# Optimization experiments

Hardware: AMD Instinct MI355X
Metric: run time of the kernel (lower is better)

The kernel has to match this reference:

```python
import jax, jax.numpy as jnp
import numpy as np

NUM_HEAD = 8
HIDDEN = 128
INPUT_DIM = 256
N1 = 1024
N2 = 1024
BATCH = 16


def setup_inputs() -> dict:
    key = jax.random.key(0)
    ks = jax.random.split(key, 10)
    HD = HIDDEN * NUM_HEAD  # 1024
    return {
        "x1": jax.random.normal(ks[0], (BATCH, N1, INPUT_DIM), jnp.float32),
        "x2": jax.random.normal(ks[1], (BATCH, N2, INPUT_DIM), jnp.float32),
        "B": jax.random.normal(ks[2], (N1, N2), jnp.float32),
        "wq_w": jax.random.normal(ks[3], (HD, INPUT_DIM), jnp.float32) * 0.02,
        "wq_b": jnp.zeros((HD,), jnp.float32),
        "wk_w": jax.random.normal(ks[4], (HD, INPUT_DIM), jnp.float32) * 0.02,
        "wk_b": jnp.zeros((HD,), jnp.float32),
        "wv_w": jax.random.normal(ks[5], (HD, INPUT_DIM), jnp.float32) * 0.02,
        "wv_b": jnp.zeros((HD,), jnp.float32),
        "proj_w": jax.random.normal(ks[6], (HIDDEN, HD), jnp.float32) * 0.02,
        "proj_b": jnp.zeros((HIDDEN,), jnp.float32),
    }


def reference(x1, x2, B, wq_w, wq_b, wk_w, wk_b, wv_w, wv_b, proj_w, proj_b):
    b, n1, _ = x1.shape
    n2 = x2.shape[1]
    sdk = jnp.sqrt(jnp.asarray(HIDDEN, x1.dtype))
    # Linear layers (torch convention: y = x @ W.T + b)
    q = x1 @ wq_w.T + wq_b                      # [b, n1, H*D]
    k = x2 @ wk_w.T + wk_b                      # [b, n2, H*D]
    v = x2 @ wv_w.T + wv_b                      # [b, n2, H*D]
    q = q.reshape(b, n1, NUM_HEAD, HIDDEN)
    k = k.reshape(b, n2, NUM_HEAD, HIDDEN)
    v = v.reshape(b, n2, NUM_HEAD, HIDDEN)
    # scores: [b, h, n1, n2]
    scores = jnp.einsum("bnhd,bmhd->bhnm", q, k) / sdk + B[None, None, :, :]
    attn = jax.nn.softmax(scores, axis=-1)
    out = jnp.einsum("bhnm,bmhd->bnhd", attn, v).reshape(b, n1, NUM_HEAD * HIDDEN)
    return out @ proj_w.T + proj_b              # [b, n1, HIDDEN]
```

## Files before the change

### kernel.cpp

```cpp
#include <hip/hip_runtime.h>
#include <hip/hip_fp16.h>

typedef _Float16 f16;
typedef __attribute__((ext_vector_type(4))) _Float16 f16x4;
typedef __attribute__((ext_vector_type(8))) _Float16 f16x8;
typedef __attribute__((ext_vector_type(4))) float f32x4;

#define MFMA_F16(a,b,c) __builtin_amdgcn_mfma_f32_16x16x32_f16((a),(b),(c),0,0,0)

__device__ __forceinline__ void gl_lds16(const f16* g, f16* l) {
  __builtin_amdgcn_global_load_lds(
      (const __attribute__((address_space(1))) unsigned int*)g,
      (__attribute__((address_space(3))) unsigned int*)l, 16, 0, 0);
}


__global__ __launch_bounds__(256) void conv_pack(
    const float* __restrict__ x1, const float* __restrict__ x2,
    const float* __restrict__ wq, const float* __restrict__ wk,
    const float* __restrict__ wv,
    f16* __restrict__ x1p, f16* __restrict__ x2p, f16* __restrict__ wp) {
  __shared__ f16 S[128][264];
  const int id = blockIdx.x, tid = threadIdx.x;
  const float* src;
  f16* dst;
  if (id < 128) {
    src = x1 + (size_t)id * 32768; dst = x1p + (size_t)id * 32768;
  } else if (id < 256) {
    src = x2 + (size_t)(id - 128) * 32768; dst = x2p + (size_t)(id - 128) * 32768;
  } else {
    const int wsel = (id - 256) >> 3, wt = (id - 256) & 7;
    const float* wsrc = (wsel == 0) ? wq : (wsel == 1) ? wk : wv;
    src = wsrc + (size_t)wt * 32768;
    dst = wp + (size_t)wsel * 262144 + (size_t)wt * 32768;
  }
#pragma unroll 8
  for (int i = 0; i < 32; i++) {
    int f = i * 256 + tid;
    int row = f >> 6, c4 = f & 63;
    float4 v = *(const float4*)(src + (size_t)row * 256 + c4 * 4);
    f16x4 hh; hh[0] = (f16)v.x; hh[1] = (f16)v.y; hh[2] = (f16)v.z; hh[3] = (f16)v.w;
    *(f16x4*)&S[row][c4 * 4] = hh;
  }
  __syncthreads();
#pragma unroll 8
  for (int i = 0; i < 16; i++) {
    int u = i * 256 + tid;
    int chunk = u >> 6, l2 = u & 63;
    int q = l2 >> 4, c = l2 & 15;
    int row = (chunk >> 3) * 16 + c, k = (chunk & 7) * 32 + q * 8;
    f16x8 v = *(const f16x8*)&S[row][k];
    *(f16x8*)(dst + (size_t)u * 8) = v;
  }
}

__global__ __launch_bounds__(256) void pack_eb(
    const float* __restrict__ Bm, f16* __restrict__ Ebp) {
  __shared__ float S[128][68];
  const int id = blockIdx.x, tid = threadIdx.x;
  const int mt = id >> 4, t = id & 15;
  const int m0 = mt * 128, n0 = t * 64;
#pragma unroll
  for (int i = 0; i < 8; i++) {
    int f = i * 256 + tid;
    int r = f >> 4, c4 = f & 15;
    float4 v = *(const float4*)(Bm + (size_t)(m0 + r) * 1024 + n0 + c4 * 4);
    *(float4*)&S[r][c4 * 4] = v;
  }
  __syncthreads();
#pragma unroll
  for (int i = 0; i < 2; i++) {
    int s = i * 256 + tid;
    int qcw = s >> 6, lane = s & 63;
    int col = lane & 15, quad = lane >> 4;
    int row = qcw * 16 + col;
    f16x8 h0, h1;
#pragma unroll
    for (int j = 0; j < 8; j++) {
      int jt = j >> 2, r = j & 3;
      h0[j] = (f16)__expf(S[row][jt * 16 + quad * 4 + r]);
    }
#pragma unroll
    for (int j = 0; j < 8; j++) {
      int jt = 2 + (j >> 2), r = j & 3;
      h1[j] = (f16)__expf(S[row][jt * 16 + quad * 4 + r]);
    }
    f16* out = Ebp + ((size_t)(id * 8 + qcw) * 2) * 512 + lane * 8;
    *(f16x8*)out = h0;
    *(f16x8*)(out + 512) = h1;
  }
}

__global__ __launch_bounds__(512) __attribute__((amdgpu_waves_per_eu(4, 4)))
void gemm_qkv(const f16* __restrict__ x1p, const f16* __restrict__ x2p,
              const f16* __restrict__ wp,
              const float* __restrict__ wqb, const float* __restrict__ wkb,
              const float* __restrict__ wvb,
              f16* __restrict__ Qp, f16* __restrict__ Kp, f16* __restrict__ Vp,
              float qscale) {
  __shared__ f16 Wl[2][8192];
  __shared__ f16 Xl[2][8192];
  const int z = blockIdx.z;
  const f16* Xp = (z == 0) ? x1p : x2p;
  const float* bias = (z == 0) ? wqb : (z == 1) ? wkb : wvb;
  f16* outp = (z == 0) ? Qp : (z == 1) ? Kp : Vp;
  const float sc = (z == 0) ? qscale : 1.0f;

  const int tid = threadIdx.x, lane = tid & 63, wid = tid >> 6;
  const int col = lane & 15, quad = lane >> 4;
  const int xt = blockIdx.x, h = blockIdx.y;
  const int wr = wid >> 2, xc = wid & 3;
  const f16* Xb = Xp + (size_t)xt * 32768;
  const f16* Wb = wp + (size_t)z * 262144 + (size_t)h * 32768;

#define QISSUE(T, bufi)                                                   \
  {                                                                       \
    _Pragma("unroll") for (int j = 0; j < 2; j++) {                       \
      int lc = wid * 2 + j;                                               \
      int rt = lc >> 1, ksl = lc & 1;                                     \
      gl_lds16(Wb + (size_t)((rt * 8 + (T) * 2 + ksl) << 9) + lane * 8,   \
               &Wl[bufi][lc * 512]);                                      \
      gl_lds16(Xb + (size_t)((rt * 8 + (T) * 2 + ksl) << 9) + lane * 8,   \
               &Xl[bufi][lc * 512]);                                      \
    }                                                                     \
  }

  QISSUE(0, 0);
  QISSUE(1, 1);

  f32x4 acc[4][2];
#pragma unroll
  for (int i = 0; i < 4; i++)
#pragma unroll
    for (int j = 0; j < 2; j++) acc[i][j] = (f32x4){0.f, 0.f, 0.f, 0.f};

  __syncthreads();

  for (int t = 0; t < 4; ++t) {
    const int buf = t & 1;
    const f16* Ra = (z == 2) ? Xl[buf] : Wl[buf];
    const f16* Cb = (z == 2) ? Wl[buf] : Xl[buf];
#pragma unroll
    for (int ksl = 0; ksl < 2; ksl++) {
      f16x8 af[4], bf[2];
#pragma unroll
      for (int i = 0; i < 4; i++)
        af[i] = *(const f16x8*)&Ra[((wr * 4 + i) * 2 + ksl) * 512 + lane * 8];
#pragma unroll
      for (int j = 0; j < 2; j++)
        bf[j] = *(const f16x8*)&Cb[((xc * 2 + j) * 2 + ksl) * 512 + lane * 8];
#pragma unroll
      for (int i = 0; i < 4; i++)
#pragma unroll
        for (int j = 0; j < 2; j++) acc[i][j] = MFMA_F16(af[i], bf[j], acc[i][j]);
    }
    __syncthreads();
    if (t + 2 < 4) QISSUE(t + 2, buf);
  }

  if (z < 2) {
#pragma unroll
    for (int i = 0; i < 4; i++) {
      const int k0h = wr * 64 + i * 16 + quad * 4;
      float4 bq = *(const float4*)(bias + h * 128 + k0h);
      const int ks2 = k0h >> 5, q2 = (k0h >> 3) & 3, lo = k0h & 7;
#pragma unroll
      for (int j = 0; j < 2; j++) {
        const int bn2 = xt * 128 + xc * 32 + j * 16 + col;
        const int b = bn2 >> 10, n2 = bn2 & 1023;
        const int T = n2 >> 6, jt = (n2 >> 4) & 3, c2 = n2 & 15;
        f16x4 pk;
#pragma unroll
        for (int r = 0; r < 4; r++)
          pk[r] = (f16)((acc[i][j][r] + ((const float*)&bq)[r]) * sc);
        *(f16x4*)(outp + (size_t)(b * 8 + h) * 131072 + T * 8192 +
                  (jt * 4 + ks2) * 512 + (q2 * 16 + c2) * 8 + lo) = pk;
      }
    }
  } else {
#pragma unroll
    for (int j = 0; j < 2; j++) {
      const int d = xc * 32 + j * 16 + col;
      const float bv = bias[h * 128 + d];
      const int ct = d >> 4, cc = d & 15;
#pragma unroll
      for (int i = 0; i < 4; i++) {
        const int bn2 = xt * 128 + wr * 64 + i * 16 + quad * 4;
        const int b = bn2 >> 10, n2 = bn2 & 1023;
        const int T = n2 >> 6, kv6 = n2 & 63;
        const int ks2 = kv6 >> 5, qv = (kv6 >> 3) & 3, jj = kv6 & 7;
        f16x4 pk;
#pragma unroll
        for (int r = 0; r < 4; r++) pk[r] = (f16)(acc[i][j][r] + bv);
        *(f16x4*)(outp + (size_t)(b * 8 + h) * 131072 + T * 8192 +
                  (ct * 2 + ks2) * 512 + (qv * 16 + cc) * 8 + jj) = pk;
      }
    }
  }
}

__global__ __launch_bounds__(256) void gemm_proj(const f16* __restrict__ A,
                                                 const float* __restrict__ W,
                                                 const float* __restrict__ bias,
                                                 float* __restrict__ out) {
  constexpr int LD = 72;
  __shared__ f16 As[64][LD];
  __shared__ f16 Bs[64][LD];
  const int tid = threadIdx.x, lane = tid & 63, wid = tid >> 6;
  const int col = lane & 15, quad = lane >> 4;
  const int wm = (wid >> 1) * 32, wn = (wid & 1) * 32;
  const int m0 = blockIdx.x * 64, n0 = blockIdx.y * 64;

  f32x4 acc[2][2];
#pragma unroll
  for (int i = 0; i < 2; i++)
#pragma unroll
    for (int j = 0; j < 2; j++) acc[i][j] = (f32x4){0.f, 0.f, 0.f, 0.f};

  for (int kt = 0; kt < 16; ++kt) {
    const int k0 = kt * 64;
#pragma unroll
    for (int i = 0; i < 2; i++) {
      int f = i * 256 + tid;
      int r = f >> 3, ch = f & 7;
      *(f16x8*)&As[r][ch * 8] = *(const f16x8*)(A + (size_t)(m0 + r) * 1024 + k0 + ch * 8);
    }
#pragma unroll
    for (int i = 0; i < 4; i++) {
      int f = i * 256 + tid;
      int r = f >> 4, c4 = f & 15;
      float4 v = *(const float4*)(W + (size_t)(n0 + r) * 1024 + k0 + c4 * 4);
      f16x4 hh; hh[0] = (f16)v.x; hh[1] = (f16)v.y; hh[2] = (f16)v.z; hh[3] = (f16)v.w;
      *(f16x4*)&Bs[r][c4 * 4] = hh;
    }
    __syncthreads();
#pragma unroll
    for (int ks = 0; ks < 2; ks++) {
      f16x8 af[2], bf[2];
#pragma unroll
      for (int i = 0; i < 2; i++) af[i] = *(const f16x8*)&As[wm + i * 16 + col][ks * 32 + quad * 8];
#pragma unroll
      for (int j = 0; j < 2; j++) bf[j] = *(const f16x8*)&Bs[wn + j * 16 + col][ks * 32 + quad * 8];
#pragma unroll
      for (int i = 0; i < 2; i++)
#pragma unroll
        for (int j = 0; j < 2; j++) acc[i][j] = MFMA_F16(af[i], bf[j], acc[i][j]);
    }
    __syncthreads();
  }
#pragma unroll
  for (int j = 0; j < 2; j++) {
    const int c = n0 + wn + j * 16 + col;
    const float bv = bias[c];
#pragma unroll
    for (int i = 0; i < 2; i++) {
      const int r0 = m0 + wm + i * 16 + quad * 4;
#pragma unroll
      for (int r = 0; r < 4; r++)
        out[(size_t)(r0 + r) * 128 + c] = acc[i][j][r] + bv;
    }
  }
}

__global__ __launch_bounds__(512, 2)
void attn_fused(const f16* __restrict__ Qp, const f16* __restrict__ Kp,
                const f16* __restrict__ Vp, const f16* __restrict__ Ebp,
                f16* __restrict__ O) {
  __shared__ f16 Ksl[2][8192];
  __shared__ f16 Vtl[2][8192];
  __shared__ f16 Ps[16384];
  const int tid = threadIdx.x, lane = tid & 63, wid = tid >> 6;
  const int col = lane & 15, quad = lane >> 4;
  const int id = blockIdx.x;
  const int mt = (id >> 3) & 3;
  const int bh = ((id >> 5) << 3) | (id & 7);
  const int b = bh >> 3, h = bh & 7;
  const int m0 = mt * 256;
  const int wm = wid * 32;

  const f16* Qb = Qp + (size_t)bh * 131072;
  const f16* Kb = Kp + (size_t)bh * 131072;
  const f16* Vb = Vp + (size_t)bh * 131072;
  const int tile128 = mt * 2 + (wid >> 2);
  const f16* Ebw = Ebp +
      (((size_t)tile128 * 16 * 8 + (wid & 3) * 2) * 2) * 512 + lane * 8;

#define AISSUE(T, bufi)                                                       \
  {                                                                           \
    if (wid < 4) {                                                            \
      _Pragma("unroll") for (int j = 0; j < 4; j++)                           \
          gl_lds16(Kb + (size_t)(T) * 8192 + (wid * 4 + j) * 512 + lane * 8,  \
                   &Ksl[bufi][(wid * 4 + j) * 512]);                          \
    } else {                                                                  \
      _Pragma("unroll") for (int j = 0; j < 4; j++)                           \
          gl_lds16(Vb + (size_t)(T) * 8192 + ((wid - 4) * 4 + j) * 512 + lane * 8, \
                   &Vtl[bufi][((wid - 4) * 4 + j) * 512]);                    \
    }                                                                         \
  }

  AISSUE(0, 0);
  AISSUE(1, 1);

  f16x8 qf[2][4];
#pragma unroll
  for (int qc = 0; qc < 2; qc++) {
    const int m = m0 + wm + qc * 16;
    const int T = m >> 6, jt2 = (m >> 4) & 3;
#pragma unroll
    for (int ks = 0; ks < 4; ks++)
      qf[qc][ks] = *(const f16x8*)(Qb + T * 8192 + (jt2 * 4 + ks) * 512 + lane * 8);
  }

  f32x4 oacc[2][8];
  float l[2] = {0.f, 0.f};
#pragma unroll
  for (int qc = 0; qc < 2; qc++)
#pragma unroll
    for (int ct = 0; ct < 8; ct++) oacc[qc][ct] = (f32x4){0.f, 0.f, 0.f, 0.f};

  __syncthreads();

  for (int t = 0; t < 16; ++t) {
    const int buf = t & 1;

    f16x8 ebA[2], ebB[2];
    {
      const f16* Et = Ebw + (size_t)t * 8192;
      ebA[0] = *(const f16x8*)(Et);
      ebB[0] = *(const f16x8*)(Et + 512);
      ebA[1] = *(const f16x8*)(Et + 1024);
      ebB[1] = *(const f16x8*)(Et + 1536);
    }

    f32x4 s[2][4];
#pragma unroll
    for (int qc = 0; qc < 2; qc++)
#pragma unroll
      for (int jt = 0; jt < 4; jt++) s[qc][jt] = (f32x4){0.f, 0.f, 0.f, 0.f};
#pragma unroll
    for (int ks = 0; ks < 4; ks++) {
      f16x8 kf[4];
#pragma unroll
      for (int jt = 0; jt < 4; jt++)
        kf[jt] = *(const f16x8*)&Ksl[buf][(jt * 4 + ks) * 512 + lane * 8];
#pragma unroll
      for (int jt = 0; jt < 4; jt++)
#pragma unroll
        for (int qc = 0; qc < 2; qc++)
          s[qc][jt] = MFMA_F16(kf[jt], qf[qc][ks], s[qc][jt]);
    }

#pragma unroll
    for (int qc = 0; qc < 2; qc++) {
      const int m = wm + qc * 16 + col;
#pragma unroll
      for (int jt = 0; jt < 4; jt++) {
        float p0, p1, p2, p3;
        if (jt < 2) {
          p0 = __expf(s[qc][jt][0]) * (float)ebA[qc][(jt & 1) * 4 + 0];
          p1 = __expf(s[qc][jt][1]) * (float)ebA[qc][(jt & 1) * 4 + 1];
          p2 = __expf(s[qc][jt][2]) * (float)ebA[qc][(jt & 1) * 4 + 2];
          p3 = __expf(s[qc][jt][3]) * (float)ebA[qc][(jt & 1) * 4 + 3];
        } else {
          p0 = __expf(s[qc][jt][0]) * (float)ebB[qc][(jt & 1) * 4 + 0];
          p1 = __expf(s[qc][jt][1]) * (float)ebB[qc][(jt & 1) * 4 + 1];
          p2 = __expf(s[qc][jt][2]) * (float)ebB[qc][(jt & 1) * 4 + 2];
          p3 = __expf(s[qc][jt][3]) * (float)ebB[qc][(jt & 1) * 4 + 3];
        }
        l[qc] += (p0 + p1) + (p2 + p3);
        f16x4 pk; pk[0] = (f16)p0; pk[1] = (f16)p1; pk[2] = (f16)p2; pk[3] = (f16)p3;
        const int g = (jt * 2 + (quad >> 1)) ^ (col & 7);
        *(f16x4*)&Ps[m * 64 + g * 8 + (quad & 1) * 4] = pk;
      }
    }

#pragma unroll
    for (int ks = 0; ks < 2; ks++) {
      f16x8 pf[2];
#pragma unroll
      for (int qc = 0; qc < 2; qc++) {
        const int m = wm + qc * 16 + col;
        const int g = (ks * 4 + quad) ^ (col & 7);
        pf[qc] = *(const f16x8*)&Ps[m * 64 + g * 8];
      }
#pragma unroll
      for (int ct = 0; ct < 8; ct++) {
        f16x8 vf = *(const f16x8*)&Vtl[buf][(ct * 2 + ks) * 512 + lane * 8];
#pragma unroll
        for (int qc = 0; qc < 2; qc++)
          oacc[qc][ct] = MFMA_F16(pf[qc], vf, oacc[qc][ct]);
      }
    }

    __syncthreads();
    if (t + 2 < 16) AISSUE(t + 2, buf);
  }

#pragma unroll
  for (int qc = 0; qc < 2; qc++) {
    float lw = l[qc];
    lw += __shfl_xor(lw, 16);
    lw += __shfl_xor(lw, 32);
    f16* Ob = O + ((size_t)(b * 1024 + m0 + wm + qc * 16)) * 1024 + h * 128;
#pragma unroll
    for (int r = 0; r < 4; r++) {
      const float lv = __shfl(lw, (lane & 48) | (quad * 4 + r));
      const float inv = 1.0f / lv;
#pragma unroll
      for (int ct = 0; ct < 8; ct++)
        Ob[(size_t)(quad * 4 + r) * 1024 + ct * 16 + col] = (f16)(oacc[qc][ct][r] * inv);
    }
  }
}

extern "C" void kernel_launch(void* const* d_in, const int* in_sizes, int n_in,
                              void* d_out, int out_size, void* d_ws, size_t ws_size,
                              hipStream_t stream) {
  (void)in_sizes; (void)n_in; (void)out_size; (void)ws_size;
  const float* x1  = (const float*)d_in[0];
  const float* x2  = (const float*)d_in[1];
  const float* Bm  = (const float*)d_in[2];
  const float* wq  = (const float*)d_in[3];
  const float* wqb = (const float*)d_in[4];
  const float* wk  = (const float*)d_in[5];
  const float* wkb = (const float*)d_in[6];
  const float* wv  = (const float*)d_in[7];
  const float* wvb = (const float*)d_in[8];
  const float* pw  = (const float*)d_in[9];
  const float* pb  = (const float*)d_in[10];
  float* out = (float*)d_out;

  const size_t MiB = 1024 * 1024;
  f16* Qp  = (f16*)d_ws;
  f16* Kp  = (f16*)((char*)d_ws + 32 * MiB);
  f16* Vp  = (f16*)((char*)d_ws + 64 * MiB);
  f16* Ow  = (f16*)((char*)d_ws + 96 * MiB);
  f16* x1p = (f16*)((char*)d_ws + 96 * MiB);
  f16* x2p = (f16*)((char*)d_ws + 104 * MiB);
  f16* wp  = (f16*)((char*)d_ws + 112 * MiB);
  f16* Ebp = (f16*)d_out;

  const float scale = 0.0883883476483184f;
  conv_pack<<<dim3(280), dim3(256), 0, stream>>>(x1, x2, wq, wk, wv, x1p, x2p, wp);
  pack_eb<<<dim3(128), dim3(256), 0, stream>>>(Bm, Ebp);
  gemm_qkv<<<dim3(128, 8, 3), dim3(512), 0, stream>>>(x1p, x2p, wp, wqb, wkb, wvb,
                                                      Qp, Kp, Vp, scale);
  attn_fused<<<dim3(512), dim3(512), 0, stream>>>(Qp, Kp, Vp, Ebp, Ow);
  gemm_proj<<<dim3(256, 2), dim3(256), 0, stream>>>(Ow, pw, pb, out);
}
```

Baseline: 262.4 us.

## Keep attention probabilities in registers by permuting K and bias layouts

Permutes the key row ordering in the packed K layout and the exp(B) packing so that the MFMA output fragment of QK^T lines up with the A-operand layout needed for the PV MFMA. This removes the LDS staging buffer for P, along with its stores, loads and swizzle. The occupancy hint changes from launch_bounds min-blocks to amdgpu_waves_per_eu(4). The change depends on the K permutation matching the V ordering, since PV sums over keys and a mismatch would silently give wrong results.

Measured after the change: 713.1 us. 172% more time.

```diff
diff --git a/kernel.cpp b/kernel.cpp
--- a/kernel.cpp
+++ b/kernel.cpp
@@ -76,15 +76,11 @@
     int row = qcw * 16 + col;
     f16x8 h0, h1;
 #pragma unroll
-    for (int j = 0; j < 8; j++) {
-      int jt = j >> 2, r = j & 3;
-      h0[j] = (f16)__expf(S[row][jt * 16 + quad * 4 + r]);
-    }
-#pragma unroll
-    for (int j = 0; j < 8; j++) {
-      int jt = 2 + (j >> 2), r = j & 3;
-      h1[j] = (f16)__expf(S[row][jt * 16 + quad * 4 + r]);
-    }
+    for (int j = 0; j < 8; j++)
+      h0[j] = (f16)__expf(S[row][quad * 8 + j]);
+#pragma unroll
+    for (int j = 0; j < 8; j++)
+      h1[j] = (f16)__expf(S[row][32 + quad * 8 + j]);
     f16* out = Ebp + ((size_t)(id * 8 + qcw) * 2) * 512 + lane * 8;
     *(f16x8*)out = h0;
     *(f16x8*)(out + 512) = h1;
@@ -168,7 +164,15 @@
       for (int j = 0; j < 2; j++) {
         const int bn2 = xt * 128 + xc * 32 + j * 16 + col;
         const int b = bn2 >> 10, n2 = bn2 & 1023;
-        const int T = n2 >> 6, jt = (n2 >> 4) & 3, c2 = n2 & 15;
+        const int T = n2 >> 6;
+        int jt, c2;
+        if (z == 1) {
+          jt = 2 * ((n2 >> 5) & 1) + ((n2 >> 2) & 1);
+          c2 = ((n2 >> 3) & 3) * 4 + (n2 & 3);
+        } else {
+          jt = (n2 >> 4) & 3;
+          c2 = n2 & 15;
+        }
         f16x4 pk;
 #pragma unroll
         for (int r = 0; r < 4; r++)
@@ -262,13 +266,12 @@
   }
 }
 
-__global__ __launch_bounds__(512, 2)
+__global__ __launch_bounds__(512) __attribute__((amdgpu_waves_per_eu(4)))
 void attn_fused(const f16* __restrict__ Qp, const f16* __restrict__ Kp,
                 const f16* __restrict__ Vp, const f16* __restrict__ Ebp,
                 f16* __restrict__ O) {
   __shared__ f16 Ksl[2][8192];
   __shared__ f16 Vtl[2][8192];
-  __shared__ f16 Ps[16384];
   const int tid = threadIdx.x, lane = tid & 63, wid = tid >> 6;
   const int col = lane & 15, quad = lane >> 4;
   const int id = blockIdx.x;
@@ -350,9 +353,9 @@
           s[qc][jt] = MFMA_F16(kf[jt], qf[qc][ks], s[qc][jt]);
     }
 
+    f16x8 pa[2][2];
 #pragma unroll
     for (int qc = 0; qc < 2; qc++) {
-      const int m = wm + qc * 16 + col;
 #pragma unroll
       for (int jt = 0; jt < 4; jt++) {
         float p0, p1, p2, p3;
@@ -369,26 +372,18 @@
         }
         l[qc] += (p0 + p1) + (p2 + p3);
         f16x4 pk; pk[0] = (f16)p0; pk[1] = (f16)p1; pk[2] = (f16)p2; pk[3] = (f16)p3;
-        const int g = (jt * 2 + (quad >> 1)) ^ (col & 7);
-        *(f16x4*)&Ps[m * 64 + g * 8 + (quad & 1) * 4] = pk;
+        ((f16x4*)&pa[qc][jt >> 1])[jt & 1] = pk;
       }
     }
 
 #pragma unroll
     for (int ks = 0; ks < 2; ks++) {
-      f16x8 pf[2];
-#pragma unroll
-      for (int qc = 0; qc < 2; qc++) {
-        const int m = wm + qc * 16 + col;
-        const int g = (ks * 4 + quad) ^ (col & 7);
-        pf[qc] = *(const f16x8*)&Ps[m * 64 + g * 8];
-      }
 #pragma unroll
       for (int ct = 0; ct < 8; ct++) {
         f16x8 vf = *(const f16x8*)&Vtl[buf][(ct * 2 + ks) * 512 + lane * 8];
 #pragma unroll
         for (int qc = 0; qc < 2; qc++)
-          oacc[qc][ct] = MFMA_F16(pf[qc], vf, oacc[qc][ct]);
+          oacc[qc][ct] = MFMA_F16(pa[qc][ks], vf, oacc[qc][ct]);
       }
     }
 
```
